# Kernel optimization log

Measured on AMD Instinct MI355X. Metric: run time of the kernel, lower is better.

The kernel has to match this reference:

```python
import jax, jax.numpy as jnp
import numpy as np

INPUT_DIM = 2048
N_EXPERTS = 64
K = 2


def setup_inputs() -> dict:
    key = jax.random.key(0)
    kx, kw, kb = jax.random.split(key, 3)
    x = jax.random.normal(kx, (4, 4096, INPUT_DIM), dtype=jnp.float32)
    # nn.Linear(input_dim, n_experts): weight [n_experts, input_dim], bias [n_experts]
    bound = 1.0 / np.sqrt(INPUT_DIM)
    W = jax.random.uniform(kw, (N_EXPERTS, INPUT_DIM), minval=-bound, maxval=bound, dtype=jnp.float32)
    b = jax.random.uniform(kb, (N_EXPERTS,), minval=-bound, maxval=bound, dtype=jnp.float32)
    return {"x": x, "W": W, "b": b}


def reference(x, W, b):
    # logits: [B, S, E]
    logits = jnp.einsum('bsd,ed->bse', x, W) + b
    topk_vals, topk_indices = jax.lax.top_k(logits, K)  # over last (expert) axis
    gate_probs = jax.nn.softmax(topk_vals, axis=-1)
    return gate_probs, topk_indices
```

## Files before the change

### kernel.cpp

```cpp
#include <hip/hip_runtime.h>
#include <math.h>
#include <stdint.h>

typedef _Float16 half8 __attribute__((ext_vector_type(8)));
typedef float floatx4 __attribute__((ext_vector_type(4)));

#define NTOK 16384
#define DIM  2048
#define NEXP 64
#define MB   64
#define NBLK (NTOK / MB)
#define KSPL 8
#define KW   (DIM / KSPL)
#define NCH  (KW / 32)
#define WSW_H8 16384
#define WSW_BYTES (2 * WSW_H8 * 16)

#define SLOT_B  8192
#define WAVE_B  (2 * SLOT_B)
#define ARING_B (8 * WAVE_B)
#define FIN_F   (64 * 65)

__global__ void wprep_kernel(const float* __restrict__ W, _Float16* __restrict__ wsw) {
    const int id   = blockIdx.x * blockDim.x + threadIdx.x;
    const int lane = id & 63;
    const int tg   = (id >> 6) & 3;
    const int sg   = id >> 8;
    const int e    = tg * 16 + (lane & 15);
    const int k    = sg * 32 + (lane >> 4) * 8;
    const float* src = W + (size_t)e * DIM + k;
    half8 h, l;
#pragma unroll
    for (int j = 0; j < 8; j++) {
        const float v  = src[j];
        const _Float16 hh = (_Float16)v;
        h[j] = hh;
        l[j] = (_Float16)((v - (float)hh) * 2048.0f);
    }
    const size_t slot = (size_t)(sg * 4 + tg) * 64 + lane;
    ((half8*)wsw)[slot]          = h;
    ((half8*)wsw)[WSW_H8 + slot] = l;
}

__device__ __forceinline__ void split_a(const float4& v0, const float4& v1,
                                        half8& hi, half8& lo) {
    const float av[8] = {v0.x, v0.y, v0.z, v0.w, v1.x, v1.y, v1.z, v1.w};
#pragma unroll
    for (int j = 0; j < 8; j++) {
        const _Float16 hh = (_Float16)av[j];
        hi[j] = hh;
        lo[j] = (_Float16)((av[j] - (float)hh) * 2048.0f);
    }
}

__device__ __forceinline__ void dma16(const void* g, const char* l) {
    __builtin_amdgcn_global_load_lds(
        (const __attribute__((address_space(1))) unsigned int*)(uintptr_t)g,
        (__attribute__((address_space(3))) unsigned int*)(uintptr_t)l,
        16, 0, 0);
}

template <int N>
__device__ __forceinline__ void wait_vm() {
    asm volatile("s_waitcnt vmcnt(%0)" :: "n"(N) : "memory");
}

template <bool USE_WS>
__global__ __launch_bounds__(512, 2)
void gating_kernel(const float* __restrict__ x, const float* __restrict__ W,
                   const _Float16* __restrict__ wsw, const float* __restrict__ bias,
                   float* __restrict__ out)
{
    __shared__ char  aring[ARING_B];
    __shared__ float fin[FIN_F];
    __shared__ float bsh[NEXP];

    const int tid  = threadIdx.x;
    const int lane = tid & 63;
    const int ks   = tid >> 6;
    const int col  = lane & 15;
    const int quad = lane >> 4;
    const int tok0 = blockIdx.x * MB;

    if (tid < NEXP) bsh[tid] = bias[tid];

    const int arow = lane >> 3;
    const int agp  = (lane & 7) ^ arow;
    const float* gA = x + (size_t)(tok0 + arow) * DIM + ks * KW + agp * 4;
    char* const wbase = aring + ks * WAVE_B;

    floatx4 accm[4][4], accl[4][4];
#pragma unroll
    for (int m = 0; m < 4; m++)
#pragma unroll
        for (int t = 0; t < 4; t++) { accm[m][t] = (floatx4){0,0,0,0}; accl[m][t] = (floatx4){0,0,0,0}; }

#pragma unroll
    for (int i = 0; i < 8; i++)
        dma16(gA + (size_t)i * 8 * DIM, wbase + i * 1024);

#pragma unroll
    for (int c = 0; c < NCH; ++c) {
        const int sg = ks * NCH + c;
        half8  bh[4], bl[4];
        float4 bf0[4], bf1[4];
        if constexpr (USE_WS) {
#pragma unroll
            for (int t = 0; t < 4; t++) {
                bh[t] = ((const half8*)wsw)[(size_t)(sg * 4 + t) * 64 + lane];
                bl[t] = ((const half8*)wsw)[WSW_H8 + (size_t)(sg * 4 + t) * 64 + lane];
            }
        } else {
#pragma unroll
            for (int t = 0; t < 4; t++) {
                const float* wr = W + (size_t)(t * 16 + col) * DIM + sg * 32 + quad * 8;
                bf0[t] = *(const float4*)wr;
                bf1[t] = *(const float4*)(wr + 4);
            }
        }
        asm volatile("" ::: "memory");
        if (c + 1 < NCH) {
#pragma unroll
            for (int i = 0; i < 8; i++)
                dma16(gA + (size_t)i * 8 * DIM + (c + 1) * 32,
                      wbase + ((c + 1) & 1) * SLOT_B + i * 1024);
        }
        asm volatile("" ::: "memory");
        if (c + 1 < NCH) wait_vm<16>();
        else             wait_vm<8>();
        asm volatile("" ::: "memory");

        const char* Ab = wbase + (c & 1) * SLOT_B;
#pragma unroll
        for (int m = 0; m < 4; m++) {
            const int row = m * 16 + col;
            const float4 v0 = *(const float4*)(Ab + row * 128 + (((2 * quad + 0) ^ (col & 7))) * 16);
            const float4 v1 = *(const float4*)(Ab + row * 128 + (((2 * quad + 1) ^ (col & 7))) * 16);
            half8 ah, al;
            split_a(v0, v1, ah, al);
#pragma unroll
            for (int t = 0; t < 4; t++) {
                half8 hb, lb;
                if constexpr (USE_WS) { hb = bh[t]; lb = bl[t]; }
                else                  { split_a(bf0[t], bf1[t], hb, lb); }
                accm[m][t] = __builtin_amdgcn_mfma_f32_16x16x32_f16(ah, hb, accm[m][t], 0, 0, 0);
                accl[m][t] = __builtin_amdgcn_mfma_f32_16x16x32_f16(ah, lb, accl[m][t], 0, 0, 0);
                accl[m][t] = __builtin_amdgcn_mfma_f32_16x16x32_f16(al, hb, accl[m][t], 0, 0, 0);
            }
        }
    }

    __syncthreads();
    {
        float* slab = (float*)(aring + ks * 16384);
        const float inv = 1.0f / 2048.0f;
#pragma unroll
        for (int m = 0; m < 4; m++)
#pragma unroll
            for (int t = 0; t < 4; t++)
#pragma unroll
                for (int r = 0; r < 4; r++)
                    slab[(m * 16 + quad * 4 + r) * 64 + t * 16 + col] =
                        accm[m][t][r] + accl[m][t][r] * inv;
    }
    __syncthreads();
    {
        const int tk = tid >> 3;
        const int e0 = (tid & 7) * 8;
        floatx4 s0 = {0,0,0,0}, s1 = {0,0,0,0};
#pragma unroll
        for (int p = 0; p < KSPL; p++) {
            const float* sb = (const float*)(aring + p * 16384) + tk * 64 + e0;
            s0 += *(const floatx4*)sb;
            s1 += *(const floatx4*)(sb + 4);
        }
#pragma unroll
        for (int j = 0; j < 4; j++) {
            fin[tk * 65 + e0 + j]     = s0[j] + bsh[e0 + j];
            fin[tk * 65 + e0 + 4 + j] = s1[j] + bsh[e0 + 4 + j];
        }
    }
    __syncthreads();

    if (tid < MB) {
        const int tk = tid;
        float v0 = -INFINITY, v1 = -INFINITY;
        int   i0 = 0, i1 = 0;
        for (int e = 0; e < NEXP; e++) {
            const float v = fin[tk * 65 + e];
            if (v > v0)      { v1 = v0; i1 = i0; v0 = v; i0 = e; }
            else if (v > v1) { v1 = v; i1 = e; }
        }
        const float e1 = expf(v1 - v0);
        const float sden = 1.f + e1;
        const int   g  = tok0 + tk;
        out[2 * g + 0] = 1.f / sden;
        out[2 * g + 1] = e1 / sden;
        out[2 * NTOK + 2 * g + 0] = (float)i0;
        out[2 * NTOK + 2 * g + 1] = (float)i1;
    }
}

extern "C" void kernel_launch(void* const* d_in, const int* in_sizes, int n_in,
                              void* d_out, int out_size, void* d_ws, size_t ws_size,
                              hipStream_t stream) {
    const float* x    = (const float*)d_in[0];
    const float* W    = (const float*)d_in[1];
    const float* bias = (const float*)d_in[2];
    float*       out  = (float*)d_out;
    _Float16*    wsw  = (_Float16*)d_ws;

    if (ws_size >= (size_t)WSW_BYTES) {
        hipLaunchKernelGGL(wprep_kernel, dim3(64), dim3(256), 0, stream, W, wsw);
        hipLaunchKernelGGL((gating_kernel<true>), dim3(NBLK), dim3(512), 0, stream,
                           x, W, wsw, bias, out);
    } else {
        hipLaunchKernelGGL((gating_kernel<false>), dim3(NBLK), dim3(512), 0, stream,
                           x, W, nullptr, bias, out);
    }
}
```

Measured before the change: 203.6 us.

## Cooperative block-wide x staging with interleaved K ownership per wave

```diff
diff --git a/kernel.cpp b/kernel.cpp
--- a/kernel.cpp
+++ b/kernel.cpp
@@ -8,18 +8,16 @@
 #define NTOK 16384
 #define DIM  2048
 #define NEXP 64
-#define MB   64
-#define NBLK (NTOK / MB)
-#define KSPL 8
-#define KW   (DIM / KSPL)
-#define NCH  (KW / 32)
+#define TPB  64
+#define NBLK (NTOK / TPB)
+#define SCK  256
+#define NSC  (DIM / SCK)
 #define WSW_H8 16384
 #define WSW_BYTES (2 * WSW_H8 * 16)
 
-#define SLOT_B  8192
-#define WAVE_B  (2 * SLOT_B)
-#define ARING_B (8 * WAVE_B)
-#define FIN_F   (64 * 65)
+#define SLOT_B 65536
+#define RING_B (2 * SLOT_B)
+#define FIN_F  (TPB * 65)
 
 __global__ void wprep_kernel(const float* __restrict__ W, _Float16* __restrict__ wsw) {
     const int id   = blockIdx.x * blockDim.x + threadIdx.x;
@@ -65,29 +63,36 @@
     asm volatile("s_waitcnt vmcnt(%0)" :: "n"(N) : "memory");
 }
 
+__device__ __forceinline__ void fence_order() {
+    asm volatile("" ::: "memory");
+}
+
 template <bool USE_WS>
 __global__ __launch_bounds__(512, 2)
 void gating_kernel(const float* __restrict__ x, const float* __restrict__ W,
                    const _Float16* __restrict__ wsw, const float* __restrict__ bias,
                    float* __restrict__ out)
 {
-    __shared__ char  aring[ARING_B];
+    __shared__ char  aring[RING_B];
     __shared__ float fin[FIN_F];
     __shared__ float bsh[NEXP];
 
     const int tid  = threadIdx.x;
     const int lane = tid & 63;
-    const int ks   = tid >> 6;
+    const int w    = tid >> 6;
     const int col  = lane & 15;
     const int quad = lane >> 4;
-    const int tok0 = blockIdx.x * MB;
+    const int tok0 = blockIdx.x * TPB;
 
     if (tid < NEXP) bsh[tid] = bias[tid];
 
-    const int arow = lane >> 3;
-    const int agp  = (lane & 7) ^ arow;
-    const float* gA = x + (size_t)(tok0 + arow) * DIM + ks * KW + agp * 4;
-    char* const wbase = aring + ks * WAVE_B;
+#pragma unroll
+    for (int i = 0; i < 8; i++) {
+        const int rw = w * 8 + i;
+        dma16(x + (size_t)(tok0 + rw) * DIM + ((lane ^ (rw & 7)) << 2),
+              aring + rw * 1024);
+    }
+    fence_order();
 
     floatx4 accm[4][4], accl[4][4];
 #pragma unroll
@@ -96,12 +101,8 @@
         for (int t = 0; t < 4; t++) { accm[m][t] = (floatx4){0,0,0,0}; accl[m][t] = (floatx4){0,0,0,0}; }
 
 #pragma unroll
-    for (int i = 0; i < 8; i++)
-        dma16(gA + (size_t)i * 8 * DIM, wbase + i * 1024);
-
-#pragma unroll
-    for (int c = 0; c < NCH; ++c) {
-        const int sg = ks * NCH + c;
+    for (int sc = 0; sc < NSC; ++sc) {
+        const int sg = sc * 8 + w;
         half8  bh[4], bl[4];
         float4 bf0[4], bf1[4];
         if constexpr (USE_WS) {
@@ -118,24 +119,28 @@
                 bf1[t] = *(const float4*)(wr + 4);
             }
         }
-        asm volatile("" ::: "memory");
-        if (c + 1 < NCH) {
-#pragma unroll
-            for (int i = 0; i < 8; i++)
-                dma16(gA + (size_t)i * 8 * DIM + (c + 1) * 32,
-                      wbase + ((c + 1) & 1) * SLOT_B + i * 1024);
-        }
-        asm volatile("" ::: "memory");
-        if (c + 1 < NCH) wait_vm<16>();
-        else             wait_vm<8>();
-        asm volatile("" ::: "memory");
-
-        const char* Ab = wbase + (c & 1) * SLOT_B;
+        fence_order();
+        wait_vm<8>();
+        __builtin_amdgcn_s_barrier();
+        fence_order();
+        if (sc + 1 < NSC) {
+#pragma unroll
+            for (int i = 0; i < 8; i++) {
+                const int rw = w * 8 + i;
+                dma16(x + (size_t)(tok0 + rw) * DIM + (sc + 1) * SCK + ((lane ^ (rw & 7)) << 2),
+                      aring + ((sc + 1) & 1) * SLOT_B + rw * 1024);
+            }
+            fence_order();
+        }
+
+        const char* Ab = aring + (sc & 1) * SLOT_B;
 #pragma unroll
         for (int m = 0; m < 4; m++) {
             const int row = m * 16 + col;
-            const float4 v0 = *(const float4*)(Ab + row * 128 + (((2 * quad + 0) ^ (col & 7))) * 16);
-            const float4 v1 = *(const float4*)(Ab + row * 128 + (((2 * quad + 1) ^ (col & 7))) * 16);
+            const int pz0 = (w * 8 + quad * 2 + 0) ^ (col & 7);
+            const int pz1 = (w * 8 + quad * 2 + 1) ^ (col & 7);
+            const float4 v0 = *(const float4*)(Ab + row * 1024 + pz0 * 16);
+            const float4 v1 = *(const float4*)(Ab + row * 1024 + pz1 * 16);
             half8 ah, al;
             split_a(v0, v1, ah, al);
 #pragma unroll
@@ -152,7 +157,7 @@
 
     __syncthreads();
     {
-        float* slab = (float*)(aring + ks * 16384);
+        float* slab = (float*)(aring + w * 16384);
         const float inv = 1.0f / 2048.0f;
 #pragma unroll
         for (int m = 0; m < 4; m++)
@@ -169,7 +174,7 @@
         const int e0 = (tid & 7) * 8;
         floatx4 s0 = {0,0,0,0}, s1 = {0,0,0,0};
 #pragma unroll
-        for (int p = 0; p < KSPL; p++) {
+        for (int p = 0; p < 8; p++) {
             const float* sb = (const float*)(aring + p * 16384) + tk * 64 + e0;
             s0 += *(const floatx4*)sb;
             s1 += *(const floatx4*)(sb + 4);
@@ -182,7 +187,7 @@
     }
     __syncthreads();
 
-    if (tid < MB) {
+    if (tid < TPB) {
         const int tk = tid;
         float v0 = -INFINITY, v1 = -INFINITY;
         int   i0 = 0, i1 = 0;
```

Result: slower. 213.5 us (+4.8%).
